# Kernel optimization log

Measured on AMD Instinct MI355X. Metric: run time of the kernel, lower is better.

## Reference

```python
import jax, jax.numpy as jnp
import numpy as np

TEMPERATURE = 0.5
EPS = 1e-8  # torch.nn.CosineSimilarity eps


def _l2norm(x):
    # torch cosine sim divides by max(||x||, eps) per vector
    n = jnp.sqrt(jnp.sum(x * x, axis=-1, keepdims=True))
    return x / jnp.maximum(n, EPS)


def setup_inputs() -> dict:
    key = jax.random.key(0)
    ka, kb = jax.random.split(key)
    batch_a = jax.random.normal(ka, (4096, 512), dtype=jnp.float32)
    batch_b = jax.random.normal(kb, (4096, 512), dtype=jnp.float32)
    return {"batch_a": batch_a, "batch_b": batch_b}


def reference(batch_a, batch_b):
    a = _l2norm(batch_a)  # [N, D]
    b = _l2norm(batch_b)
    inv_t = 1.0 / TEMPERATURE
    # cosine similarity via normalize + GEMM (same math as broadcast mul+reduce)
    sim11 = (a @ a.T) * inv_t  # [N, N]
    sim22 = (b @ b.T) * inv_t
    sim12 = (a @ b.T) * inv_t
    n = sim12.shape[-1]
    eye = jnp.eye(n, dtype=bool)
    neg_inf = jnp.float32(-jnp.inf)
    sim11 = jnp.where(eye, neg_inf, sim11)
    sim22 = jnp.where(eye, neg_inf, sim22)
    # logits: [[sim12, sim11], [sim22, sim12^T]] -> [2N, 2N]
    logits = jnp.concatenate(
        [jnp.concatenate([sim12, sim11], axis=-1),
         jnp.concatenate([sim22, sim12.T], axis=-1)],
        axis=-2,
    )
    targets = jnp.arange(2 * n)
    logp = jax.nn.log_softmax(logits, axis=-1)  # stable single pass
    loss = -jnp.mean(logp[jnp.arange(2 * n), targets])
    return loss
```

## Files before the change

kernel.cpp:

```cpp
#include <hip/hip_runtime.h>

#define NR 4096
#define DD 512
#define TWO_N 8192
#define MT 64
#define NTILES 2080
#define CHUNK 260

using bf16x8 = __attribute__((ext_vector_type(8))) short;
using f32x4  = __attribute__((ext_vector_type(4))) float;

__device__ __forceinline__ unsigned short f2bf(float f) {
    union { float f; unsigned u; } v; v.f = f;
    unsigned r = v.u + 0x7fff + ((v.u >> 16) & 1);
    return (unsigned short)(r >> 16);
}

__global__ __launch_bounds__(256) void ntx_nrm_kernel(const float* __restrict__ A,
                                                      const float* __restrict__ B,
                                                      unsigned short* __restrict__ X,
                                                      float* __restrict__ d12,
                                                      float* __restrict__ S) {
    const int row = blockIdx.x;
    const int t = threadIdx.x;
    const int lane = t & 63, wid = t >> 6;

    if (t < 2) S[row * 2 + t] = 0.f;

    const float2 av = *(const float2*)(A + row * DD + 2 * t);
    const float2 bv = *(const float2*)(B + row * DD + 2 * t);
    float sa = av.x * av.x + av.y * av.y;
    float sb = bv.x * bv.x + bv.y * bv.y;
#pragma unroll
    for (int o = 32; o; o >>= 1) { sa += __shfl_down(sa, o); sb += __shfl_down(sb, o); }

    __shared__ float red[12];
    if (lane == 0) { red[wid] = sa; red[4 + wid] = sb; }
    __syncthreads();
    const float ta = red[0] + red[1] + red[2] + red[3];
    const float tb = red[4] + red[5] + red[6] + red[7];
    const float ra = 1.f / fmaxf(sqrtf(ta), 1e-8f);
    const float rb = 1.f / fmaxf(sqrtf(tb), 1e-8f);
    const float nax = av.x * ra, nay = av.y * ra;
    const float nbx = bv.x * rb, nby = bv.y * rb;

    *(unsigned*)(X + row * DD + 2 * t) =
        (unsigned)f2bf(nax) | ((unsigned)f2bf(nay) << 16);
    *(unsigned*)(X + (NR + row) * DD + 2 * t) =
        (unsigned)f2bf(nbx) | ((unsigned)f2bf(nby) << 16);

    float dt = nax * nbx + nay * nby;
#pragma unroll
    for (int o = 32; o; o >>= 1) dt += __shfl_down(dt, o);
    if (lane == 0) red[8 + wid] = dt;
    __syncthreads();
    if (t == 0) d12[row] = red[8] + red[9] + red[10] + red[11];
}

__global__ __launch_bounds__(256) void ntx_gemm_lse_kernel(const unsigned short* __restrict__ X,
                                                           float* __restrict__ S) {
    const int bid = blockIdx.x;
    const int sid = (bid & 7) * CHUNK + (bid >> 3);
    int u, v;
    if (sid < 1792) {
        const int s = sid >> 6, loc = sid & 63;
        int U = 0;
        while (7 * (U + 1) - (U + 1) * U / 2 <= s) ++U;
        const int V = U + 1 + (s - (7 * U - U * (U - 1) / 2));
        u = U * 8 + (loc >> 3);
        v = V * 8 + (loc & 7);
    } else {
        const int s2 = sid - 1792;
        const int U = s2 / 36, loc = s2 % 36;
        int lu = 0;
        while ((lu + 1) * 8 - (lu + 1) * lu / 2 <= loc) ++lu;
        const int lv = lu + (loc - (lu * 8 - lu * (lu - 1) / 2));
        u = U * 8 + lu;
        v = U * 8 + lv;
    }
    const bool fixedTile = (u == v);
    const int rowTile = u * 128, colTile = (v ^ 32) * 128;

    __shared__ unsigned short As[2][128 * 64];
    __shared__ unsigned short Bs[2][128 * 64];

    const int t = threadIdx.x;
    const int lane = t & 63, wid = t >> 6;
    const int waveRow = wid >> 1, waveCol = wid & 1;
    const int lr = lane & 15, grp = lane >> 4;
    const int r3 = lr & 7;

    f32x4 acc[4][4] = {};

    const int srow = lane >> 3;
    const int scol = ((lane & 7) ^ srow) * 8;

    auto STAGE = [&](int sel, int kt) {
#pragma unroll
        for (int q = 0; q < 4; ++q) {
            const int ci = wid * 4 + q;
            const int r  = ci * 8 + srow;
            const int lo = ci * 512 + lane * 8;
            __builtin_amdgcn_global_load_lds(
                (const __attribute__((address_space(1))) unsigned*)(X + (size_t)(rowTile + r) * DD + kt + scol),
                (__attribute__((address_space(3))) unsigned*)&As[sel][lo], 16, 0, 0);
            __builtin_amdgcn_global_load_lds(
                (const __attribute__((address_space(1))) unsigned*)(X + (size_t)((colTile + r) ^ NR) * DD + kt + scol),
                (__attribute__((address_space(3))) unsigned*)&Bs[sel][lo], 16, 0, 0);
        }
    };

    auto COMPUTE = [&](int sel) {
#pragma unroll
        for (int kk = 0; kk < 2; ++kk) {
            bf16x8 af[4], bfr[4];
#pragma unroll
            for (int m = 0; m < 4; ++m)
                af[m] = *(const bf16x8*)&As[sel][(waveRow * 64 + m * 16 + lr) * 64 +
                                                 (((kk * 4 + grp) ^ r3) * 8)];
#pragma unroll
            for (int n = 0; n < 4; ++n)
                bfr[n] = *(const bf16x8*)&Bs[sel][(waveCol * 64 + n * 16 + lr) * 64 +
                                                  (((kk * 4 + grp) ^ r3) * 8)];
#pragma unroll
            for (int m = 0; m < 4; ++m)
#pragma unroll
                for (int n = 0; n < 4; ++n)
                    acc[m][n] = __builtin_amdgcn_mfma_f32_16x16x32_bf16(af[m], bfr[n], acc[m][n], 0, 0, 0);
        }
    };

    STAGE(0, 0);
    STAGE(1, 64);
#pragma unroll
    for (int i = 0; i < 8; ++i) {
        const int cur = i & 1;
        if (i < 7) asm volatile("s_waitcnt vmcnt(8)" ::: "memory");
        else       asm volatile("s_waitcnt vmcnt(0)" ::: "memory");
        __builtin_amdgcn_s_barrier();
        COMPUTE(cur);
        if (i < 6) {
            asm volatile("s_waitcnt lgkmcnt(0)" ::: "memory");
            __builtin_amdgcn_s_barrier();
            STAGE(cur, (i + 2) * 64);
        }
    }

#pragma unroll
    for (int m = 0; m < 4; ++m)
#pragma unroll
        for (int n = 0; n < 4; ++n)
#pragma unroll
            for (int reg = 0; reg < 4; ++reg) {
                const int R = rowTile + waveRow * 64 + m * 16 + grp * 4 + reg;
                const int C = colTile + waveCol * 64 + n * 16 + lr;
                const bool masked = fixedTile && (C == (R ^ NR));
                acc[m][n][reg] = masked ? 0.f : __expf(acc[m][n][reg] * 2.0f);
            }

#pragma unroll
    for (int m = 0; m < 4; ++m)
#pragma unroll
        for (int reg = 0; reg < 4; ++reg) {
            float rs = acc[m][0][reg] + acc[m][1][reg] + acc[m][2][reg] + acc[m][3][reg];
            rs += __shfl_xor(rs, 1);
            rs += __shfl_xor(rs, 2);
            rs += __shfl_xor(rs, 4);
            rs += __shfl_xor(rs, 8);
            if (lr == 0) {
                const int R = rowTile + waveRow * 64 + m * 16 + grp * 4 + reg;
                atomicAdd(&S[R], rs);
            }
        }

    if (!fixedTile) {
#pragma unroll
        for (int n = 0; n < 4; ++n) {
            float cs = 0.f;
#pragma unroll
            for (int m = 0; m < 4; ++m)
#pragma unroll
                for (int reg = 0; reg < 4; ++reg)
                    cs += acc[m][n][reg];
            cs += __shfl_xor(cs, 16);
            cs += __shfl_xor(cs, 32);
            if (grp == 0) {
                const int C = colTile + waveCol * 64 + n * 16 + lr;
                atomicAdd(&S[C ^ NR], cs);
            }
        }
    }
}

__global__ __launch_bounds__(256) void ntx_loss_kernel(const float* __restrict__ S,
                                                       const float* __restrict__ d12,
                                                       float* __restrict__ out) {
    const int t = threadIdx.x;
    float a = 0.f;
    for (int r = t; r < TWO_N; r += 256)
        a += __logf(S[r]) - 2.0f * d12[r & (NR - 1)];
    const int lane = t & 63, wid = t >> 6;
#pragma unroll
    for (int o = 32; o; o >>= 1) a += __shfl_down(a, o);
    __shared__ float red[4];
    if (lane == 0) red[wid] = a;
    __syncthreads();
    if (t == 0) out[0] = (red[0] + red[1] + red[2] + red[3]) * (1.f / (float)TWO_N);
}

extern "C" void kernel_launch(void* const* d_in, const int* in_sizes, int n_in,
                              void* d_out, int out_size, void* d_ws, size_t ws_size,
                              hipStream_t stream) {
    const float* A = (const float*)d_in[0];
    const float* B = (const float*)d_in[1];

    unsigned short* X = (unsigned short*)d_ws;
    float* S   = (float*)((char*)d_ws + (size_t)TWO_N * DD * 2);
    float* d12 = (float*)((char*)S + (size_t)TWO_N * 4);

    ntx_nrm_kernel<<<NR, 256, 0, stream>>>(A, B, X, d12, S);

    ntx_gemm_lse_kernel<<<NTILES, 256, 0, stream>>>(X, S);

    ntx_loss_kernel<<<1, 256, 0, stream>>>(S, d12, (float*)d_out);
}
```

Baseline: 81.56 us.

## Quantize normalized embeddings to FP8 and use scaled f8f6f4 MFMA for similarity GEMM

The normalization kernel now writes the normalized rows as FP8 (e4m3) instead of bf16. The GEMM uses the MI355X mfma_scale 16x16x128 f8f6f4 instruction with unit scales, which halves operand bytes and the number of K iterations. The LDS tiles are resized and the swizzle is adjusted to 16-byte chunks. The final loss kernel is also spread over 32 blocks that combine results with atomicAdd after a memset. The lower precision risks accuracy error in the exponentiated logits, which are scaled by 1/T=2.

```diff
diff --git a/kernel.cpp b/kernel.cpp
--- a/kernel.cpp
+++ b/kernel.cpp
@@ -7,18 +7,12 @@
 #define NTILES 2080
 #define CHUNK 260
 
-using bf16x8 = __attribute__((ext_vector_type(8))) short;
-using f32x4  = __attribute__((ext_vector_type(4))) float;
-
-__device__ __forceinline__ unsigned short f2bf(float f) {
-    union { float f; unsigned u; } v; v.f = f;
-    unsigned r = v.u + 0x7fff + ((v.u >> 16) & 1);
-    return (unsigned short)(r >> 16);
-}
+using f32x4 = __attribute__((ext_vector_type(4))) float;
+using i32x8 = __attribute__((ext_vector_type(8))) int;
 
 __global__ __launch_bounds__(256) void ntx_nrm_kernel(const float* __restrict__ A,
                                                       const float* __restrict__ B,
-                                                      unsigned short* __restrict__ X,
+                                                      unsigned char* __restrict__ X8,
                                                       float* __restrict__ d12,
                                                       float* __restrict__ S) {
     const int row = blockIdx.x;
@@ -44,10 +38,10 @@
     const float nax = av.x * ra, nay = av.y * ra;
     const float nbx = bv.x * rb, nby = bv.y * rb;
 
-    *(unsigned*)(X + row * DD + 2 * t) =
-        (unsigned)f2bf(nax) | ((unsigned)f2bf(nay) << 16);
-    *(unsigned*)(X + (NR + row) * DD + 2 * t) =
-        (unsigned)f2bf(nbx) | ((unsigned)f2bf(nby) << 16);
+    const unsigned pa = __builtin_amdgcn_cvt_pk_fp8_f32(nax, nay, 0, false);
+    const unsigned pb = __builtin_amdgcn_cvt_pk_fp8_f32(nbx, nby, 0, false);
+    *(unsigned short*)(X8 + (size_t)row * DD + 2 * t) = (unsigned short)pa;
+    *(unsigned short*)(X8 + (size_t)(NR + row) * DD + 2 * t) = (unsigned short)pb;
 
     float dt = nax * nbx + nay * nby;
 #pragma unroll
@@ -57,7 +51,7 @@
     if (t == 0) d12[row] = red[8] + red[9] + red[10] + red[11];
 }
 
-__global__ __launch_bounds__(256) void ntx_gemm_lse_kernel(const unsigned short* __restrict__ X,
+__global__ __launch_bounds__(256) void ntx_gemm_lse_kernel(const unsigned char* __restrict__ X8,
                                                            float* __restrict__ S) {
     const int bid = blockIdx.x;
     const int sid = (bid & 7) * CHUNK + (bid >> 3);
@@ -81,8 +75,8 @@
     const bool fixedTile = (u == v);
     const int rowTile = u * 128, colTile = (v ^ 32) * 128;
 
-    __shared__ unsigned short As[2][128 * 64];
-    __shared__ unsigned short Bs[2][128 * 64];
+    __shared__ unsigned char As[2][128 * 128];
+    __shared__ unsigned char Bs[2][128 * 128];
 
     const int t = threadIdx.x;
     const int lane = t & 63, wid = t >> 6;
@@ -93,56 +87,63 @@
     f32x4 acc[4][4] = {};
 
     const int srow = lane >> 3;
-    const int scol = ((lane & 7) ^ srow) * 8;
-
-    auto STAGE = [&](int sel, int kt) {
+    const int scol = ((lane & 7) ^ srow) * 16;
+
+    auto STAGE = [&](int sel, int kb) {
 #pragma unroll
         for (int q = 0; q < 4; ++q) {
             const int ci = wid * 4 + q;
             const int r  = ci * 8 + srow;
-            const int lo = ci * 512 + lane * 8;
+            const int lo = ci * 1024 + lane * 16;
             __builtin_amdgcn_global_load_lds(
-                (const __attribute__((address_space(1))) unsigned*)(X + (size_t)(rowTile + r) * DD + kt + scol),
+                (const __attribute__((address_space(1))) unsigned*)(X8 + (size_t)(rowTile + r) * DD + kb + scol),
                 (__attribute__((address_space(3))) unsigned*)&As[sel][lo], 16, 0, 0);
             __builtin_amdgcn_global_load_lds(
-                (const __attribute__((address_space(1))) unsigned*)(X + (size_t)((colTile + r) ^ NR) * DD + kt + scol),
+                (const __attribute__((address_space(1))) unsigned*)(X8 + (size_t)((colTile + r) ^ NR) * DD + kb + scol),
                 (__attribute__((address_space(3))) unsigned*)&Bs[sel][lo], 16, 0, 0);
         }
     };
 
     auto COMPUTE = [&](int sel) {
-#pragma unroll
-        for (int kk = 0; kk < 2; ++kk) {
-            bf16x8 af[4], bfr[4];
-#pragma unroll
-            for (int m = 0; m < 4; ++m)
-                af[m] = *(const bf16x8*)&As[sel][(waveRow * 64 + m * 16 + lr) * 64 +
-                                                 (((kk * 4 + grp) ^ r3) * 8)];
+        i32x8 a8[4], b8[4];
+#pragma unroll
+        for (int m = 0; m < 4; ++m) {
+            const int rb = (waveRow * 64 + m * 16 + lr) * 128;
+            const int4 lo = *(const int4*)&As[sel][rb + (((grp * 2 + 0) ^ r3) * 16)];
+            const int4 hi = *(const int4*)&As[sel][rb + (((grp * 2 + 1) ^ r3) * 16)];
+            a8[m][0] = lo.x; a8[m][1] = lo.y; a8[m][2] = lo.z; a8[m][3] = lo.w;
+            a8[m][4] = hi.x; a8[m][5] = hi.y; a8[m][6] = hi.z; a8[m][7] = hi.w;
+        }
+#pragma unroll
+        for (int n = 0; n < 4; ++n) {
+            const int rb = (waveCol * 64 + n * 16 + lr) * 128;
+            const int4 lo = *(const int4*)&Bs[sel][rb + (((grp * 2 + 0) ^ r3) * 16)];
+            const int4 hi = *(const int4*)&Bs[sel][rb + (((grp * 2 + 1) ^ r3) * 16)];
+            b8[n][0] = lo.x; b8[n][1] = lo.y; b8[n][2] = lo.z; b8[n][3] = lo.w;
+            b8[n][4] = hi.x; b8[n][5] = hi.y; b8[n][6] = hi.z; b8[n][7] = hi.w;
+        }
+#pragma unroll
+        for (int m = 0; m < 4; ++m)
 #pragma unroll
             for (int n = 0; n < 4; ++n)
-                bfr[n] = *(const bf16x8*)&Bs[sel][(waveCol * 64 + n * 16 + lr) * 64 +
-                                                  (((kk * 4 + grp) ^ r3) * 8)];
-#pragma unroll
-            for (int m = 0; m < 4; ++m)
-#pragma unroll
-                for (int n = 0; n < 4; ++n)
-                    acc[m][n] = __builtin_amdgcn_mfma_f32_16x16x32_bf16(af[m], bfr[n], acc[m][n], 0, 0, 0);
-        }
+                acc[m][n] = __builtin_amdgcn_mfma_scale_f32_16x16x128_f8f6f4(
+                    a8[m], b8[n], acc[m][n], 0 , 0 ,
+                    0, 0x7F7F7F7F, 0, 0x7F7F7F7F);
     };
 
     STAGE(0, 0);
-    STAGE(1, 64);
-#pragma unroll
-    for (int i = 0; i < 8; ++i) {
+    STAGE(1, 128);
+#pragma unroll
+    for (int i = 0; i < 4; ++i) {
         const int cur = i & 1;
-        if (i < 7) asm volatile("s_waitcnt vmcnt(8)" ::: "memory");
+        if (i < 3) asm volatile("s_waitcnt vmcnt(8)" ::: "memory");
         else       asm volatile("s_waitcnt vmcnt(0)" ::: "memory");
         __builtin_amdgcn_s_barrier();
         COMPUTE(cur);
-        if (i < 6) {
+        if (i < 2) {
             asm volatile("s_waitcnt lgkmcnt(0)" ::: "memory");
             __builtin_amdgcn_s_barrier();
-            STAGE(cur, (i + 2) * 64);
+            STAGE(cur, (i + 2) * 128);
         }
     }
 
@@ -196,16 +197,15 @@
                                                        const float* __restrict__ d12,
                                                        float* __restrict__ out) {
     const int t = threadIdx.x;
-    float a = 0.f;
-    for (int r = t; r < TWO_N; r += 256)
-        a += __logf(S[r]) - 2.0f * d12[r & (NR - 1)];
+    const int r = blockIdx.x * 256 + t;
+    float a = __logf(S[r]) - 2.0f * d12[r & (NR - 1)];
     const int lane = t & 63, wid = t >> 6;
 #pragma unroll
     for (int o = 32; o; o >>= 1) a += __shfl_down(a, o);
     __shared__ float red[4];
     if (lane == 0) red[wid] = a;
     __syncthreads();
-    if (t == 0) out[0] = (red[0] + red[1] + red[2] + red[3]) * (1.f / (float)TWO_N);
+    if (t == 0) atomicAdd(out, (red[0] + red[1] + red[2] + red[3]) * (1.f / (float)TWO_N));
 }
 
 extern "C" void kernel_launch(void* const* d_in, const int* in_sizes, int n_in,
@@ -214,13 +214,15 @@
     const float* A = (const float*)d_in[0];
     const float* B = (const float*)d_in[1];
 
-    unsigned short* X = (unsigned short*)d_ws;
-    float* S   = (float*)((char*)d_ws + (size_t)TWO_N * DD * 2);
+    unsigned char* X8 = (unsigned char*)d_ws;
+    float* S   = (float*)((char*)d_ws + (size_t)TWO_N * DD);
     float* d12 = (float*)((char*)S + (size_t)TWO_N * 4);
 
-    ntx_nrm_kernel<<<NR, 256, 0, stream>>>(A, B, X, d12, S);
-
-    ntx_gemm_lse_kernel<<<NTILES, 256, 0, stream>>>(X, S);
-
-    ntx_loss_kernel<<<1, 256, 0, stream>>>(S, d12, (float*)d_out);
-}
+    (void)hipMemsetAsync(d_out, 0, sizeof(float), stream);
+
+    ntx_nrm_kernel<<<NR, 256, 0, stream>>>(A, B, X8, d12, S);
+
+    ntx_gemm_lse_kernel<<<NTILES, 256, 0, stream>>>(X8, S);
+
+    ntx_loss_kernel<<<TWO_N / 256, 256, 0, stream>>>(S, d12, (float*)d_out);
+}
```

New measurement: 80.58 us. About the same (-1.2%).
